# Kernel tuning notes

Hardware: AMD Instinct MI355X
Metric: run time of the kernel (lower is better)

## Reference

```python
import jax, jax.numpy as jnp
import numpy as np

EPS = 1e-7
NCE_T = 0.07
NCE_M = 0.5

def _unit(x):
    return x / jnp.sqrt(jnp.sum(x * x, axis=-1, keepdims=True))

def setup_inputs() -> dict:
    key = jax.random.key(0)
    k1, k2, k3, k4, k5, k6 = jax.random.split(key, 6)
    B, D, K, N = 256, 128, 8192, 500000
    f_s = _unit(jax.random.normal(k1, (B, D), dtype=jnp.float32))
    f_t = _unit(jax.random.normal(k2, (B, D), dtype=jnp.float32))
    memory_v1 = _unit(jax.random.normal(k3, (N, D), dtype=jnp.float32))
    memory_v2 = _unit(jax.random.normal(k4, (N, D), dtype=jnp.float32))
    idx = jax.random.randint(k5, (B,), 0, N)
    contrast_idx = jax.random.randint(k6, (B, K), 0, N)
    return {"f_s": f_s, "f_t": f_t, "memory_v1": memory_v1,
            "memory_v2": memory_v2, "idx": idx, "contrast_idx": contrast_idx}

def _contrast_loss(x, n_data):
    # ContrastLoss (Eq 18): x is [B, K+1], col 0 = positive score
    bsz = x.shape[0]
    m = x.shape[1] - 1
    Pn = 1.0 / float(n_data)
    denom_add = m * Pn + EPS
    log_D1 = jnp.log(x[:, 0] / (x[:, 0] + denom_add))          # positives
    log_D0 = jnp.log((m * Pn) / (x[:, 1:] + denom_add))        # negatives
    return -(log_D1.sum() + log_D0.sum()) / bsz

def reference(f_s, f_t, memory_v1, memory_v2, idx, contrast_idx):
    n_data = memory_v1.shape[0]
    # full index set: positive in column 0, then K negatives
    full_idx = jnp.concatenate([idx[:, None], contrast_idx], axis=1)  # [B, K+1]
    # gather memory rows (detached in the original torch code)
    w_v1 = jax.lax.stop_gradient(memory_v1[full_idx])  # [B, K+1, D]
    w_v2 = jax.lax.stop_gradient(memory_v2[full_idx])  # [B, K+1, D]
    # per-sample dot-product scoring + temperature
    out_v2 = jnp.exp(jnp.einsum('bkd,bd->bk', w_v1, f_t) / NCE_T)
    out_v1 = jnp.exp(jnp.einsum('bkd,bd->bk', w_v2, f_s) / NCE_T)
    # Z set on first forward as mean * outputSize (a detached scalar in torch)
    Z_v1 = jax.lax.stop_gradient(out_v1.mean()) * n_data
    Z_v2 = jax.lax.stop_gradient(out_v2.mean()) * n_data
    out_v1 = out_v1 / Z_v1
    out_v2 = out_v2 / Z_v2
    # momentum scatter update of memory banks (no-grad in original)
    def update(mem, feats):
        old = mem[idx]                                   # [B, D]
        new = old * NCE_M + feats * (1.0 - NCE_M)
        new = new / jnp.sqrt(jnp.sum(new * new, axis=1, keepdims=True))
        return mem.at[idx].set(new)
    new_v1 = update(memory_v1, jax.lax.stop_gradient(f_s))
    new_v2 = update(memory_v2, jax.lax.stop_gradient(f_t))
    # out_s = out_v1 (student anchored), out_t = out_v2 (teacher anchored)
    loss = _contrast_loss(out_v1, n_data) + _contrast_loss(out_v2, n_data)
    return loss, new_v1, new_v2
```

## Files before the change

### kernel.cpp

```cpp
#include <hip/hip_runtime.h>
#include <stdint.h>

#define BB   256
#define DD   128
#define KK   8192
#define KP1  8193
#define NDATA 500000
#define MEMELEMS 64000000

__global__ __launch_bounds__(256) void score_kernel(
    const float* __restrict__ f_s, const float* __restrict__ f_t,
    const float* __restrict__ mv1, const float* __restrict__ mv2,
    const int* __restrict__ idx, const int* __restrict__ cidx,
    float* __restrict__ sA, float* __restrict__ sB, double* __restrict__ acc)
{
    const int b   = blockIdx.y;
    const int tid = threadIdx.x;
    const int g   = tid >> 4;
    const int fl  = tid & 15;

    const float4* fs4 = (const float4*)f_s;
    const float4* ft4 = (const float4*)f_t;
    const float4* m14 = (const float4*)mv1;
    const float4* m24 = (const float4*)mv2;

    const int foff = b * 32 + fl * 2;
    const float4 fsa = fs4[foff], fsb = fs4[foff + 1];
    const float4 fta = ft4[foff], ftb = ft4[foff + 1];

    const float invT = 1.0f / 0.07f;
    float accA = 0.f, accB = 0.f;
    const int kbase = blockIdx.x * 128;

    #pragma unroll
    for (int it = 0; it < 8; ++it) {
        const int k = kbase + it * 16 + g;
        if (k < KP1) {
            const int j  = (k == 0) ? idx[b] : cidx[b * KK + (k - 1)];
            const int ro = j * 32 + fl * 2;
            const float4 a1 = m14[ro], b1 = m14[ro + 1];
            const float4 a2 = m24[ro], b2 = m24[ro + 1];
            float p1 = a2.x*fsa.x + a2.y*fsa.y + a2.z*fsa.z + a2.w*fsa.w
                     + b2.x*fsb.x + b2.y*fsb.y + b2.z*fsb.z + b2.w*fsb.w;
            float p2 = a1.x*fta.x + a1.y*fta.y + a1.z*fta.z + a1.w*fta.w
                     + b1.x*ftb.x + b1.y*ftb.y + b1.z*ftb.z + b1.w*ftb.w;
            #pragma unroll
            for (int off = 1; off < 16; off <<= 1) {
                p1 += __shfl_xor(p1, off);
                p2 += __shfl_xor(p2, off);
            }
            if (fl == 0) {
                const float e1 = __expf(p1 * invT);
                const float e2 = __expf(p2 * invT);
                sA[b * KP1 + k] = e1;
                sB[b * KP1 + k] = e2;
                accA += e1;
                accB += e2;
            }
        }
    }

    __shared__ float lA[16], lB[16];
    if (fl == 0) { lA[g] = accA; lB[g] = accB; }
    __syncthreads();
    if (tid == 0) {
        float ta = 0.f, tb = 0.f;
        #pragma unroll
        for (int i = 0; i < 16; ++i) { ta += lA[i]; tb += lB[i]; }
        atomicAdd(&acc[0], (double)ta);
        atomicAdd(&acc[1], (double)tb);
    }
}

__global__ __launch_bounds__(256) void loss_kernel(
    const float* __restrict__ sA, const float* __restrict__ sB,
    const double* __restrict__ acc, double* __restrict__ lossAcc)
{
    const int b = blockIdx.y;
    const int k = blockIdx.x * 256 + threadIdx.x;

    const double denom = (double)BB * (double)KP1;
    const float invZ1 = (float)(denom / (acc[0] * (double)NDATA));
    const float invZ2 = (float)(denom / (acc[1] * (double)NDATA));
    const float mPn = (float)KK / (float)NDATA;
    const float c   = mPn + 1e-7f;

    float t = 0.f;
    if (k < KP1) {
        const float x1 = sA[b * KP1 + k] * invZ1;
        const float x2 = sB[b * KP1 + k] * invZ2;
        if (k == 0) {
            t = logf(x1 / (x1 + c)) + logf(x2 / (x2 + c));
        } else {
            t = logf(mPn / (x1 + c)) + logf(mPn / (x2 + c));
        }
    }
    #pragma unroll
    for (int off = 1; off < 64; off <<= 1) t += __shfl_xor(t, off);
    __shared__ float ls[4];
    if ((threadIdx.x & 63) == 0) ls[threadIdx.x >> 6] = t;
    __syncthreads();
    if (threadIdx.x == 0)
        atomicAdd(lossAcc, (double)(ls[0] + ls[1] + ls[2] + ls[3]));
}

__global__ void finalize_kernel(const double* __restrict__ acc,
                                float* __restrict__ out)
{
    out[0] = (float)(-acc[2] / (double)BB);
}

__global__ __launch_bounds__(128) void update_kernel(
    const float* __restrict__ mv1, const float* __restrict__ mv2,
    const float* __restrict__ f_s, const float* __restrict__ f_t,
    const int* __restrict__ idx, float* __restrict__ out)
{
    const int v = blockIdx.x >> 8;
    const int b = blockIdx.x & 255;
    const int j = idx[b];
    for (int b2 = b + 1; b2 < BB; ++b2)
        if (idx[b2] == j) return;

    const float* mem = v ? mv2 : mv1;
    const float* f   = v ? f_t : f_s;
    const int t = threadIdx.x;
    const float n = 0.5f * mem[(size_t)j * DD + t] + 0.5f * f[b * DD + t];

    float ss = n * n;
    #pragma unroll
    for (int off = 1; off < 64; off <<= 1) ss += __shfl_xor(ss, off);
    __shared__ float ls[2];
    if ((t & 63) == 0) ls[t >> 6] = ss;
    __syncthreads();
    const float total = ls[0] + ls[1];

    out[1 + (size_t)v * MEMELEMS + (size_t)j * DD + t] = n / sqrtf(total);
}

extern "C" void kernel_launch(void* const* d_in, const int* in_sizes, int n_in,
                              void* d_out, int out_size, void* d_ws, size_t ws_size,
                              hipStream_t stream)
{
    const float* f_s = (const float*)d_in[0];
    const float* f_t = (const float*)d_in[1];
    const float* mv1 = (const float*)d_in[2];
    const float* mv2 = (const float*)d_in[3];
    const int*   idx  = (const int*)d_in[4];
    const int*   cidx = (const int*)d_in[5];
    float* out = (float*)d_out;

    const size_t sElems = (size_t)BB * KP1;
    double* acc;
    float*  sA;
    if (ws_size >= 256 + 2 * sElems * sizeof(float)) {
        acc = (double*)d_ws;
        sA  = (float*)((char*)d_ws + 256);
    } else {
        uintptr_t p = (uintptr_t)(out + 1 + (size_t)MEMELEMS);
        p = (p + 255) & ~(uintptr_t)255;
        acc = (double*)p;
        sA  = (float*)(acc + 8);
    }
    float* sB = sA + sElems;

    hipMemsetAsync(acc, 0, 3 * sizeof(double), stream);

    dim3 gS(65, BB);
    score_kernel<<<gS, 256, 0, stream>>>(f_s, f_t, mv1, mv2, idx, cidx, sA, sB, acc);

    dim3 gL(33, BB);
    loss_kernel<<<gL, 256, 0, stream>>>(sA, sB, acc, &acc[2]);

    finalize_kernel<<<1, 1, 0, stream>>>(acc, out);

    hipMemcpyAsync(out + 1, mv1, (size_t)MEMELEMS * sizeof(float),
                   hipMemcpyDeviceToDevice, stream);
    hipMemcpyAsync(out + 1 + (size_t)MEMELEMS, mv2, (size_t)MEMELEMS * sizeof(float),
                   hipMemcpyDeviceToDevice, stream);
    update_kernel<<<512, 128, 0, stream>>>(mv1, mv2, f_s, f_t, idx, out);
}
```

Measured before the change: 1.552 ms.

## Fuse memory-bank copy into score kernel with aligned float4 stores

Replaces the two device-to-device memcpys of the 64M-element banks with a grid-stride float4 copy appended to the score kernel. The score grid is flattened to 1D. Because the output bank starts at out+1, the copy offsets by 3 floats so that stores are 16-byte aligned, and the few unaligned edge elements are handled separately. The intent is to overlap the bandwidth-bound copy with the gather/score work and to avoid memcpy engine overhead. In exchange, the copy loads are misaligned and register pressure in the score blocks rises.

```diff
diff --git a/kernel.cpp b/kernel.cpp
--- a/kernel.cpp
+++ b/kernel.cpp
@@ -6,16 +6,22 @@
 #define KK   8192
 #define KP1  8193
 #define NDATA 500000
-#define MEMELEMS 64000000
-
-__global__ __launch_bounds__(256) void score_kernel(
+#define MEMELEMS 64000000ULL
+#define KCHUNKS 65
+#define SCORE_BLOCKS (KCHUNKS * BB)
+#define NCHUNK 15999999ULL
+
+__global__ __launch_bounds__(256) void fused_kernel(
     const float* __restrict__ f_s, const float* __restrict__ f_t,
     const float* __restrict__ mv1, const float* __restrict__ mv2,
     const int* __restrict__ idx, const int* __restrict__ cidx,
-    float* __restrict__ sA, float* __restrict__ sB, double* __restrict__ acc)
-{
-    const int b   = blockIdx.y;
+    float* __restrict__ sA, float* __restrict__ sB, double* __restrict__ acc,
+    float* __restrict__ out1, float* __restrict__ out2, int do_copy)
+{
+    const int bid = blockIdx.x;
     const int tid = threadIdx.x;
+    const int b   = bid / KCHUNKS;
+    const int kc  = bid % KCHUNKS;
     const int g   = tid >> 4;
     const int fl  = tid & 15;
 
@@ -30,7 +36,7 @@
 
     const float invT = 1.0f / 0.07f;
     float accA = 0.f, accB = 0.f;
-    const int kbase = blockIdx.x * 128;
+    const int kbase = kc * 128;
 
     #pragma unroll
     for (int it = 0; it < 8; ++it) {
@@ -70,6 +76,25 @@
         atomicAdd(&acc[0], (double)ta);
         atomicAdd(&acc[1], (double)tb);
     }
+
+    if (do_copy) {
+        const size_t stride = (size_t)SCORE_BLOCKS * 256;
+        const float* s1 = mv1 + 3;
+        const float* s2 = mv2 + 3;
+        float4* d1 = (float4*)(out1 + 3);
+        float4* d2 = (float4*)(out2 + 3);
+        for (size_t i = (size_t)bid * 256 + tid; i < NCHUNK; i += stride) {
+            d1[i] = *(const float4*)(s1 + 4 * i);
+            d2[i] = *(const float4*)(s2 + 4 * i);
+        }
+        if (bid == 0) {
+            if (tid < 3) { out1[tid] = mv1[tid]; out2[tid] = mv2[tid]; }
+            else if (tid == 3) {
+                out1[MEMELEMS - 1] = mv1[MEMELEMS - 1];
+                out2[MEMELEMS - 1] = mv2[MEMELEMS - 1];
+            }
+        }
+    }
 }
 
 __global__ __launch_bounds__(256) void loss_kernel(
@@ -152,6 +177,7 @@
     const size_t sElems = (size_t)BB * KP1;
     double* acc;
     float*  sA;
+    int do_copy = 1;
     if (ws_size >= 256 + 2 * sElems * sizeof(float)) {
         acc = (double*)d_ws;
         sA  = (float*)((char*)d_ws + 256);
@@ -160,22 +186,28 @@
         p = (p + 255) & ~(uintptr_t)255;
         acc = (double*)p;
         sA  = (float*)(acc + 8);
+        do_copy = 0;
     }
     float* sB = sA + sElems;
 
     hipMemsetAsync(acc, 0, 3 * sizeof(double), stream);
 
-    dim3 gS(65, BB);
-    score_kernel<<<gS, 256, 0, stream>>>(f_s, f_t, mv1, mv2, idx, cidx, sA, sB, acc);
+    fused_kernel<<<SCORE_BLOCKS, 256, 0, stream>>>(
+        f_s, f_t, mv1, mv2, idx, cidx, sA, sB, acc,
+        out + 1, out + 1 + (size_t)MEMELEMS, do_copy);
 
     dim3 gL(33, BB);
     loss_kernel<<<gL, 256, 0, stream>>>(sA, sB, acc, &acc[2]);
 
     finalize_kernel<<<1, 1, 0, stream>>>(acc, out);
 
-    hipMemcpyAsync(out + 1, mv1, (size_t)MEMELEMS * sizeof(float),
-                   hipMemcpyDeviceToDevice, stream);
-    hipMemcpyAsync(out + 1 + (size_t)MEMELEMS, mv2, (size_t)MEMELEMS * sizeof(float),
-                   hipMemcpyDeviceToDevice, stream);
+    if (!do_copy) {
+        hipMemcpyAsync(out + 1, mv1, (size_t)MEMELEMS * sizeof(float),
+                       hipMemcpyDeviceToDevice, stream);
+        hipMemcpyAsync(out + 1 + (size_t)MEMELEMS, mv2,
+                       (size_t)MEMELEMS * sizeof(float),
+                       hipMemcpyDeviceToDevice, stream);
+    }
+
     update_kernel<<<512, 128, 0, stream>>>(mv1, mv2, f_s, f_t, idx, out);
 }
```

Result: faster. 1.279 ms (-17.6%).
